# Optimization experiments

Measured on AMD Instinct MI355X. Metric: run time of the kernel, lower is better.

Reference implementation:

```python
import jax, jax.numpy as jnp
import numpy as np

B, S, D, DC, H = 4, 2048, 768, 384, 12
HD = DC // H  # compressed head_dim = 32


def setup_inputs() -> dict:
    key = jax.random.key(0)
    ks = jax.random.split(key, 8)
    std = 0.02
    return {
        "hidden_states": jax.random.normal(ks[0], (B, S, D), dtype=jnp.float32),
        "W_attn": jax.random.normal(ks[1], (D, 3 * D), dtype=jnp.float32) * std,
        "b_attn": jnp.zeros((3 * D,), dtype=jnp.float32),
        "P_q": jax.random.normal(ks[2], (D, DC), dtype=jnp.float32) * std,
        "P_k": jax.random.normal(ks[3], (D, DC), dtype=jnp.float32) * std,
        "P_v": jax.random.normal(ks[4], (D, DC), dtype=jnp.float32) * std,
        "W_back": jax.random.normal(ks[5], (DC, D), dtype=jnp.float32) * std,
        "W_proj": jax.random.normal(ks[6], (D, D), dtype=jnp.float32) * std,
        "b_proj": jnp.zeros((D,), dtype=jnp.float32),
    }


def reference(hidden_states, W_attn, b_attn, P_q, P_k, P_v, W_back, W_proj, b_proj):
    b, s, _ = hidden_states.shape
    # GPT-2 Conv1D style c_attn: out = x @ W + b, then split into q,k,v
    qkv = hidden_states @ W_attn + b_attn          # [B,S,3D]
    q, k, v = jnp.split(qkv, 3, axis=-1)           # each [B,S,D]
    # sparsify hooks: per-token linear compression D -> DC
    q = q @ P_q                                    # [B,S,DC]
    k = k @ P_k
    v = v @ P_v
    # split heads -> [B,H,S,HD]
    split = lambda t: t.reshape(b, s, H, HD).transpose(0, 2, 1, 3)
    qh, kh, vh = split(q), split(k), split(v)
    # naive attention with explicit causal mask (as in original _attn)
    scores = jnp.einsum("bhqd,bhkd->bhqk", qh, kh) / jnp.sqrt(jnp.float32(HD))
    causal = jnp.tril(jnp.ones((s, s), dtype=scores.dtype))  # [S,S]
    scores = scores * causal + (-10000.0) * (1.0 - causal)
    weights = jax.nn.softmax(scores, axis=-1)
    ctx = jnp.einsum("bhqk,bhkd->bhqd", weights, vh)         # [B,H,S,HD]
    # merge heads -> [B,S,DC]
    ctx = ctx.transpose(0, 2, 1, 3).reshape(b, s, DC)
    # backproject DC -> D, then c_proj
    out = ctx @ W_back                             # [B,S,D]
    out = out @ W_proj + b_proj                    # [B,S,D]
    return out
```

## Files before the change

kernel.cpp:

```cpp
#include <hip/hip_runtime.h>
#include <math.h>


typedef unsigned short u16;
typedef unsigned int   u32;

#define VLD 8320

using short8 = __attribute__((ext_vector_type(8))) short;
using bf16x4 = __attribute__((ext_vector_type(4))) short;
using f32x4  = __attribute__((ext_vector_type(4))) float;

__device__ __forceinline__ u16 f2bf(float f) {
  u32 u = __builtin_bit_cast(u32, f);
  u = (u + 0x7fffu + ((u >> 16) & 1u)) >> 16;
  return (u16)u;
}

__device__ __forceinline__ float b2f(u16 b) {
  return __builtin_bit_cast(float, (u32)b << 16);
}

__device__ __forceinline__ u32 cvtpk_bf16(float lo, float hi) {
  u32 d;
  asm("v_cvt_pk_bf16_f32 %0, %1, %2" : "=v"(d) : "v"(lo), "v"(hi));
  return d;
}

__device__ __forceinline__ bf16x4 pack4(const f32x4 v) {
  union { u32 u[2]; bf16x4 s; } c;
  c.u[0] = cvtpk_bf16(v[0], v[1]);
  c.u[1] = cvtpk_bf16(v[2], v[3]);
  return c.s;
}

__device__ __forceinline__ float exp2v(float x) {
  return __builtin_amdgcn_exp2f(x);
}

__device__ __forceinline__ f32x4 mfma16bf(bf16x4 a, bf16x4 b, f32x4 c) {
#if __has_builtin(__builtin_amdgcn_mfma_f32_16x16x16bf16_1k)
  return __builtin_amdgcn_mfma_f32_16x16x16bf16_1k(a, b, c, 0, 0, 0);
#elif __has_builtin(__builtin_amdgcn_mfma_f32_16x16x16_bf16)
  return __builtin_amdgcn_mfma_f32_16x16x16_bf16(a, b, c, 0, 0, 0);
#else
  f32x4 d;
  asm("v_mfma_f32_16x16x16_bf16 %0, %1, %2, %3"
      : "=v"(d) : "v"(a), "v"(b), "v"(c));
  return d;
#endif
}

__device__ __forceinline__ void gload_lds16(const void* g, void* l) {
  __builtin_amdgcn_global_load_lds((__attribute__((address_space(1))) u32*)g,
                                   (__attribute__((address_space(3))) u32*)l,
                                   16, 0, 0);
}

__device__ __forceinline__ u32 lds_u32(const void* p) {
  return (u32)(size_t)(const __attribute__((address_space(3))) char*)p;
}

__global__ __launch_bounds__(256) void prep_all(
    const float* __restrict__ x, const float* __restrict__ Wa,
    const float* __restrict__ Wb, const float* __restrict__ Pq,
    const float* __restrict__ Pk, const float* __restrict__ Pv,
    const float* __restrict__ Wp,
    u16* __restrict__ x_bf, u16* __restrict__ Wat_bf, u16* __restrict__ Wbk_bf,
    u16* __restrict__ PT, u16* __restrict__ WprT) {
  __shared__ float t[32][33];
  const int blk = blockIdx.x, tid = threadIdx.x;
  if (blk < 8160) {
    const float* src; u16* dst; int i;
    if (blk < 6144)      { src = x;  dst = x_bf;   i = blk * 256 + tid; }
    else if (blk < 7872) { src = Wa; dst = Wat_bf; i = (blk - 6144) * 256 + tid; }
    else                 { src = Wb; dst = Wbk_bf; i = (blk - 7872) * 256 + tid; }
    const float4 v = ((const float4*)src)[i];
    ((ushort4*)dst)[i] = make_ushort4(f2bf(v.x), f2bf(v.y), f2bf(v.z), f2bf(v.w));
    return;
  }
  const float* src; u16* dst; int C, R, bx, by;
  if (blk < 8448)      { src = Pq; dst = PT;             R = 768; C = 384; int t2 = blk - 8160; bx = t2 % 12; by = t2 / 12; }
  else if (blk < 8736) { src = Pk; dst = PT + 384 * 768; R = 768; C = 384; int t2 = blk - 8448; bx = t2 % 12; by = t2 / 12; }
  else if (blk < 9024) { src = Pv; dst = PT + 768 * 768; R = 768; C = 384; int t2 = blk - 8736; bx = t2 % 12; by = t2 / 12; }
  else                 { src = Wp; dst = WprT;           R = 768; C = 768; int t2 = blk - 9024; bx = t2 % 24; by = t2 / 24; }
  const int c0 = bx * 32, r0 = by * 32, tx = tid & 31, ty = tid >> 5;
  for (int i = ty; i < 32; i += 8)
    t[i][tx] = src[(size_t)(r0 + i) * C + c0 + tx];
  __syncthreads();
  for (int i = ty; i < 32; i += 8)
    dst[(size_t)(c0 + i) * R + r0 + tx] = f2bf(t[tx][i]);
}

template<int OBF16>
__device__ __forceinline__ void gemm_tile(
    const u16* __restrict__ A, const u16* __restrict__ BT,
    const float* __restrict__ bias, void* __restrict__ Cv,
    int K, int lda, int ldb, int ldc, int m0, int n0, int biasmode, bool slab,
    u16* As, u16* Bs) {
  const int tid = threadIdx.x;
  const int l = tid & 63, w = tid >> 6;
  const int r = l & 15, g = l >> 4;
  const int koff = slab ? (m0 / 384) * 768 : 0;
  const u16* Ap = A + ((size_t)m0 + w * 16 + r) * lda + g * 8;
  const u16* Bp = BT + ((size_t)n0 + w * 16 + r) * ldb + koff + g * 8;
  f32x4 acc[4][4] = {};
  const int wma = (w >> 1) * 4, wnb = (w & 1) * 4;
  const int nk = K >> 5;

  const u32 abase = lds_u32(As) + (u32)(wma * 1024 + l * 16);
  const u32 bbase = lds_u32(Bs) + (u32)(wnb * 1024 + l * 16);

  auto stage = [&](int kt, int buf) {
    const int o = buf * 4096;
    gload_lds16(Ap + kt,                    &As[o + (size_t)tid * 8]);
    gload_lds16(Ap + kt + (size_t)64 * lda, &As[o + 2048 + (size_t)tid * 8]);
    gload_lds16(Bp + kt,                    &Bs[o + (size_t)tid * 8]);
    gload_lds16(Bp + kt + (size_t)64 * ldb, &Bs[o + 2048 + (size_t)tid * 8]);
  };

  stage(0, 0);
  stage(32, 1);
  stage(64, 2);
  int cur = 0;
  for (int t = 0; t < nk; ++t) {
    if (t + 2 < nk)      asm volatile("s_waitcnt vmcnt(8)" ::: "memory");
    else if (t + 1 < nk) asm volatile("s_waitcnt vmcnt(4)" ::: "memory");
    else                 asm volatile("s_waitcnt vmcnt(0)" ::: "memory");
    __builtin_amdgcn_s_barrier();
    __builtin_amdgcn_sched_barrier(0);
    const u32 off = (u32)(cur * 8192);
    short8 af[4], bfr[4];
    #pragma unroll
    for (int i = 0; i < 4; ++i) {
      asm volatile("ds_read_b128 %0, %1" : "=v"(af[i])  : "v"(abase + off + 1024u * i));
      asm volatile("ds_read_b128 %0, %1" : "=v"(bfr[i]) : "v"(bbase + off + 1024u * i));
    }
    asm volatile("s_waitcnt lgkmcnt(0)" ::: "memory");
    __builtin_amdgcn_sched_barrier(0);
    __builtin_amdgcn_s_barrier();
    __builtin_amdgcn_sched_barrier(0);
    if (t + 3 < nk) stage((t + 3) << 5, cur);
    #pragma unroll
    for (int mi = 0; mi < 4; ++mi)
      #pragma unroll
      for (int ni = 0; ni < 4; ++ni)
        acc[mi][ni] = __builtin_amdgcn_mfma_f32_16x16x32_bf16(af[mi], bfr[ni],
                                                              acc[mi][ni], 0, 0, 0);
    cur = (cur == 2) ? 0 : cur + 1;
  }

  const int row0 = m0 + (w >> 1) * 64, col0 = n0 + (w & 1) * 64;
  #pragma unroll
  for (int ni = 0; ni < 4; ++ni) {
    const int col = col0 + ni * 16 + r;
    const float bvc = (biasmode == 1) ? bias[col] : 0.f;
    #pragma unroll
    for (int mi = 0; mi < 4; ++mi)
      #pragma unroll
      for (int j = 0; j < 4; ++j) {
        const int row = row0 + mi * 16 + 4 * g + j;
        float bv = bvc;
        if (biasmode == 2) bv = bias[row];
        const float v = acc[mi][ni][j] + bv;
        if (OBF16) ((u16*)Cv)[(size_t)row * ldc + col] = f2bf(v);
        else       ((float*)Cv)[(size_t)row * ldc + col] = v;
      }
  }
}

__global__ __launch_bounds__(256, 3) void gemm_prep(
    const u16* __restrict__ PT, const u16* __restrict__ Wat,
    const u16* __restrict__ WprT, const u16* __restrict__ Wbk,
    const float* __restrict__ ba,
    u16* __restrict__ WcT, u16* __restrict__ WbpT, float* __restrict__ bc) {
  __shared__ alignas(16) u16 As[12288], Bs[12288];
  const int t = blockIdx.x;
  if (t < 54) {
    gemm_tile<1>(PT, Wat, nullptr, WcT, 768, 768, 2304, 768,
                 (t % 9) * 128, (t / 9) * 128, 0, true, As, Bs);
  } else if (t < 72) {
    const int t2 = t - 54;
    gemm_tile<1>(WprT, Wbk, nullptr, WbpT, 768, 768, 768, 384,
                 (t2 % 6) * 128, (t2 / 6) * 128, 0, false, As, Bs);
  } else {
    const int c = (t - 72) * 144 + threadIdx.x;
    if (threadIdx.x < 144 && c < 1152) {
      const int slab = c / 384;
      const float* bs = ba + slab * 768;
      const u16* row = PT + (size_t)c * 768;
      float s = 0.f;
      for (int jj = 0; jj < 96; ++jj) {
        const short8 v = *(const short8*)&row[jj * 8];
        #pragma unroll
        for (int e = 0; e < 8; ++e)
          s = fmaf(bs[jj * 8 + e], b2f((u16)v[e]), s);
      }
      bc[c] = s;
    }
  }
}

__global__ __launch_bounds__(256, 3) void gemm_qkvt(
    const u16* __restrict__ x_bf, const u16* __restrict__ WcT,
    const float* __restrict__ bc, u16* __restrict__ QKbuf, u16* __restrict__ VTbuf) {
  __shared__ alignas(16) u16 As[12288], Bs[12288];
  const int t = blockIdx.x;
  const int w = (t & 7) * 72 + (t >> 3);
  const int s = w / 9, j = w % 9;
  if (j < 6) {
    gemm_tile<1>(x_bf, WcT, bc, QKbuf, 768, 768, 768, 768,
                 s * 128, j * 128, 1, false, As, Bs);
  } else {
    gemm_tile<1>(WcT + (size_t)768 * 768, x_bf, bc + 768, VTbuf, 768, 768, 768, VLD,
                 (j - 6) * 128, s * 128, 2, false, As, Bs);
  }
}

__global__ __launch_bounds__(256, 3) void gemm_out(
    const u16* __restrict__ ctx, const u16* __restrict__ WbpT,
    const float* __restrict__ bp, float* __restrict__ out) {
  __shared__ alignas(16) u16 As[12288], Bs[12288];
  const int t = blockIdx.x;
  const int w = (t & 7) * 48 + (t >> 3);
  gemm_tile<0>(ctx, WbpT, bp, out, 384, 384, 384, 768,
               (w / 6) * 128, (w % 6) * 128, 1, false, As, Bs);
}

__global__ __launch_bounds__(256, 4) void attn_kernel(
    const u16* __restrict__ QK, const u16* __restrict__ VT,
    u16* __restrict__ ctx) {
  __shared__ alignas(16) u16 Ks[2][2048];
  __shared__ alignas(16) u16 Vs[2][32 * 72];
  const int tid = threadIdx.x;
  const int w = tid >> 6, l = tid & 63;
  const int r = l & 15, g = l >> 4;
  const int idx = blockIdx.x;
  const int cc = 15 - idx / 48;
  const int bh = idx % 48;
  const int b = bh / 12, h = bh % 12;
  const size_t tok0 = (size_t)b * 2048;
  const int q0 = cc * 128 + w * 32;
  const u16* Qb = QK + (tok0 + q0) * 768 + h * 32;
  const u16* Kb = QK + tok0 * 768 + 384 + h * 32;
  const u16* Vb = VT + (size_t)(h * 32) * VLD + b * 2048;
  const float scale2 = 0.25500526474f;
  const float THR = 8.0f;
  const f32x4 fz = {0.f, 0.f, 0.f, 0.f};

  short8 qf[2];
  qf[0] = *(const short8*)&Qb[(size_t)r * 768 + 8 * g];
  qf[1] = *(const short8*)&Qb[(size_t)(16 + r) * 768 + 8 * g];

  float mrun[2] = {-3.0e38f, -3.0e38f};
  float lpart[2] = {0.f, 0.f};
  f32x4 o[2][2] = {};
  const int ntb = 2 * (cc + 1);
  const int ntw = (q0 + 31) / 64 + 1;

  const int krow = ((tid >> 6) << 4) + (tid & 15);
  const int kcol = ((tid >> 4) & 3) * 8;
  const int vd   = tid >> 3;
  const int vkc  = (tid & 7) * 8;

  uint4 vreg;
  auto stageK = [&](int t, int buf) {
    gload_lds16(&Kb[(size_t)(t * 64 + krow) * 768 + kcol], &Ks[buf][(size_t)tid * 8]);
  };
  auto loadV = [&](int t) {
    vreg = *(const uint4*)&Vb[(size_t)vd * VLD + t * 64 + vkc];
  };
  auto writeV = [&](int buf) {
    *(uint4*)&Vs[buf][vd * 72 + vkc] = vreg;
  };

  loadV(0); stageK(0, 0); writeV(0);
  __syncthreads();
  int cur = 0;
  for (int t = 0; t < ntb; ++t) {
    const bool pf = (t + 1 < ntb);
    if (pf) { loadV(t + 1); stageK(t + 1, cur ^ 1); }
    if (t < ntw) {
      short8 kf[4];
      #pragma unroll
      for (int kj = 0; kj < 4; ++kj)
        kf[kj] = *(const short8*)&Ks[cur][((kj * 64 + l)) * 8];
      bf16x4 vf[2][4];
      #pragma unroll
      for (int di = 0; di < 2; ++di)
        #pragma unroll
        for (int kj = 0; kj < 4; ++kj)
          vf[di][kj] = *(const bf16x4*)&Vs[cur][(16 * di + r) * 72 + kj * 16 + 4 * g];

      f32x4 s[2][4];
      __builtin_amdgcn_s_setprio(1);
      #pragma unroll
      for (int kj = 0; kj < 4; ++kj)
        #pragma unroll
        for (int mi = 0; mi < 2; ++mi)
          s[mi][kj] = __builtin_amdgcn_mfma_f32_16x16x32_bf16(kf[kj], qf[mi], fz, 0, 0, 0);
      __builtin_amdgcn_s_setprio(0);

      if (t == ntw - 1) {
        #pragma unroll
        for (int mi = 0; mi < 2; ++mi) {
          const int qq = q0 + mi * 16 + r;
          #pragma unroll
          for (int kj = 0; kj < 4; ++kj)
            #pragma unroll
            for (int jj = 0; jj < 4; ++jj) {
              const int kk = t * 64 + kj * 16 + 4 * g + jj;
              if (kk > qq) s[mi][kj][jj] = -3.0e38f;
            }
        }
      }

      #pragma unroll
      for (int mi = 0; mi < 2; ++mi) {
        const float a0 = fmaxf(fmaxf(s[mi][0][0], s[mi][0][1]), fmaxf(s[mi][0][2], s[mi][0][3]));
        const float a1 = fmaxf(fmaxf(s[mi][1][0], s[mi][1][1]), fmaxf(s[mi][1][2], s[mi][1][3]));
        const float a2 = fmaxf(fmaxf(s[mi][2][0], s[mi][2][1]), fmaxf(s[mi][2][2], s[mi][2][3]));
        const float a3 = fmaxf(fmaxf(s[mi][3][0], s[mi][3][1]), fmaxf(s[mi][3][2], s[mi][3][3]));
        const float lmxs = fmaxf(fmaxf(a0, a1), fmaxf(a2, a3)) * scale2;
        if (__any(lmxs > mrun[mi] + THR)) {
          float mx = lmxs;
          mx = fmaxf(mx, __shfl_xor(mx, 16));
          mx = fmaxf(mx, __shfl_xor(mx, 32));
          const float mnew = fmaxf(mrun[mi], mx);
          const float al = exp2v(mrun[mi] - mnew);
          mrun[mi] = mnew;
          lpart[mi] *= al;
          o[0][mi] *= al;
          o[1][mi] *= al;
        }
        #pragma unroll
        for (int kj = 0; kj < 4; ++kj)
          #pragma unroll
          for (int jj = 0; jj < 4; ++jj) {
            const float pv = exp2v(fmaf(s[mi][kj][jj], scale2, -mrun[mi]));
            s[mi][kj][jj] = pv;
            lpart[mi] += pv;
          }
      }

      __builtin_amdgcn_s_setprio(1);
      #pragma unroll
      for (int kj = 0; kj < 4; ++kj) {
        const bf16x4 pf0 = pack4(s[0][kj]);
        const bf16x4 pf1 = pack4(s[1][kj]);
        #pragma unroll
        for (int di = 0; di < 2; ++di) {
          o[di][0] = mfma16bf(vf[di][kj], pf0, o[di][0]);
          o[di][1] = mfma16bf(vf[di][kj], pf1, o[di][1]);
        }
      }
      __builtin_amdgcn_s_setprio(0);
    }
    if (pf) writeV(cur ^ 1);
    __syncthreads();
    cur ^= 1;
  }

  #pragma unroll
  for (int mi = 0; mi < 2; ++mi) {
    float lr = lpart[mi];
    lr += __shfl_xor(lr, 16);
    lr += __shfl_xor(lr, 32);
    const float li = 1.0f / lr;
    const size_t row = tok0 + q0 + mi * 16 + r;
    #pragma unroll
    for (int di = 0; di < 2; ++di) {
      const u32 d0 = cvtpk_bf16(o[di][mi][0] * li, o[di][mi][1] * li);
      const u32 d1 = cvtpk_bf16(o[di][mi][2] * li, o[di][mi][3] * li);
      *(uint2*)&ctx[row * 384 + h * 32 + di * 16 + 4 * g] = make_uint2(d0, d1);
    }
  }
}

extern "C" void kernel_launch(void* const* d_in, const int* in_sizes, int n_in,
                              void* d_out, int out_size, void* d_ws, size_t ws_size,
                              hipStream_t stream) {
  const float* x      = (const float*)d_in[0];
  const float* W_attn = (const float*)d_in[1];
  const float* b_attn = (const float*)d_in[2];
  const float* P_q    = (const float*)d_in[3];
  const float* P_k    = (const float*)d_in[4];
  const float* P_v    = (const float*)d_in[5];
  const float* W_back = (const float*)d_in[6];
  const float* W_proj = (const float*)d_in[7];
  const float* b_proj = (const float*)d_in[8];

  char* ws = (char*)d_ws;
  u16*   x_bf   = (u16*)(ws);
  u16*   ctx    = (u16*)(ws);
  u16*   Wat_bf = (u16*)(ws + 12582912);
  u16*   PT     = (u16*)(ws + 16121856);
  u16*   Wbk_bf = (u16*)(ws + 17891328);
  u16*   WprT   = (u16*)(ws + 18481152);
  u16*   WcT    = (u16*)(ws + 19660800);
  u16*   WbpT   = (u16*)(ws + 21430272);
  float* bc     = (float*)(ws + 22020096);
  u16*   QKbuf  = (u16*)d_out;
  u16*   VTbuf  = (u16*)((char*)d_out + 12582912);
  float* out    = (float*)d_out;

  prep_all<<<9600, 256, 0, stream>>>(x, W_attn, W_back, P_q, P_k, P_v, W_proj,
                                     x_bf, Wat_bf, Wbk_bf, PT, WprT);
  gemm_prep<<<80, 256, 0, stream>>>(PT, Wat_bf, WprT, Wbk_bf, b_attn, WcT, WbpT, bc);
  gemm_qkvt<<<576, 256, 0, stream>>>(x_bf, WcT, bc, QKbuf, VTbuf);
  attn_kernel<<<768, 256, 0, stream>>>(QKbuf, VTbuf, ctx);
  gemm_out<<<384, 256, 0, stream>>>(ctx, WbpT, b_proj, out);
}
```

Measured before the change: 120.9 us.

## Use 512-thread 128x256 GEMM tiles with three-stage LDS pipeline for QKV and output

Adds a gemm_tile8 routine in which 8 waves compute a 128x256 output tile, each wave owning a 64x64 sub-tile. Global-to-LDS loads are triple-buffered and issued three k-steps ahead, with vmcnt-based waits. The QKV/VT projection and the output projection kernels switch to this tile with half as many 512-thread blocks, to get more data reuse per block and hide load latency better. The cost is more LDS per block (72KB) and fewer blocks to spread over the CUs, which can lower occupancy and hurt load balance.

```diff
diff --git a/kernel.cpp b/kernel.cpp
--- a/kernel.cpp
+++ b/kernel.cpp
@@ -93,7 +93,83 @@
 }
 
 template<int OBF16>
-__device__ __forceinline__ void gemm_tile(
+__device__ __forceinline__ void gemm_tile8(
+    const u16* __restrict__ A, const u16* __restrict__ BT,
+    const float* __restrict__ bias, void* __restrict__ Cv,
+    int K, int lda, int ldb, int ldc, int m0, int n0, int biasmode,
+    u16* As, u16* Bs) {
+  const int tid = threadIdx.x;
+  const int l = tid & 63, w = tid >> 6;
+  const int r = l & 15, g = l >> 4;
+  const int w8 = w;
+  const u16* Ap = A + ((size_t)m0 + w8 * 16 + r) * lda + g * 8;
+  const u16* Bp = BT + ((size_t)n0 + w8 * 16 + r) * ldb + g * 8;
+  f32x4 acc[4][4] = {};
+  const int wm = w >> 2, wn = w & 3;
+  const int nk = K >> 5;
+
+  const u32 abase = lds_u32(As) + (u32)(wm * 4096 + l * 16);
+  const u32 bbase = lds_u32(Bs) + (u32)(wn * 4096 + l * 16);
+
+  auto stage = [&](int kt, int buf) {
+    gload_lds16(Ap + kt,                     &As[buf * 4096 + (size_t)tid * 8]);
+    gload_lds16(Bp + kt,                     &Bs[buf * 8192 + (size_t)tid * 8]);
+    gload_lds16(Bp + kt + (size_t)128 * ldb, &Bs[buf * 8192 + 4096 + (size_t)tid * 8]);
+  };
+
+  stage(0, 0);
+  stage(32, 1);
+  stage(64, 2);
+  int cur = 0;
+  for (int t = 0; t < nk; ++t) {
+    if (t + 2 < nk)      asm volatile("s_waitcnt vmcnt(6)" ::: "memory");
+    else if (t + 1 < nk) asm volatile("s_waitcnt vmcnt(3)" ::: "memory");
+    else                 asm volatile("s_waitcnt vmcnt(0)" ::: "memory");
+    __builtin_amdgcn_s_barrier();
+    __builtin_amdgcn_sched_barrier(0);
+    const u32 aoff = (u32)(cur * 8192);
+    const u32 boff = (u32)(cur * 16384);
+    short8 af[4], bfr[4];
+    #pragma unroll
+    for (int i = 0; i < 4; ++i) {
+      asm volatile("ds_read_b128 %0, %1" : "=v"(af[i])  : "v"(abase + aoff + 1024u * i));
+      asm volatile("ds_read_b128 %0, %1" : "=v"(bfr[i]) : "v"(bbase + boff + 1024u * i));
+    }
+    asm volatile("s_waitcnt lgkmcnt(0)" ::: "memory");
+    __builtin_amdgcn_sched_barrier(0);
+    __builtin_amdgcn_s_barrier();
+    __builtin_amdgcn_sched_barrier(0);
+    if (t + 3 < nk) stage((t + 3) << 5, cur);
+    #pragma unroll
+    for (int mi = 0; mi < 4; ++mi)
+      #pragma unroll
+      for (int ni = 0; ni < 4; ++ni)
+        acc[mi][ni] = __builtin_amdgcn_mfma_f32_16x16x32_bf16(af[mi], bfr[ni],
+                                                              acc[mi][ni], 0, 0, 0);
+    cur = (cur == 2) ? 0 : cur + 1;
+  }
+
+  const int row0 = m0 + wm * 64, col0 = n0 + wn * 64;
+  #pragma unroll
+  for (int ni = 0; ni < 4; ++ni) {
+    const int col = col0 + ni * 16 + r;
+    const float bvc = (biasmode == 1) ? bias[col] : 0.f;
+    #pragma unroll
+    for (int mi = 0; mi < 4; ++mi)
+      #pragma unroll
+      for (int j = 0; j < 4; ++j) {
+        const int row = row0 + mi * 16 + 4 * g + j;
+        float bv = bvc;
+        if (biasmode == 2) bv = bias[row];
+        const float v = acc[mi][ni][j] + bv;
+        if (OBF16) ((u16*)Cv)[(size_t)row * ldc + col] = f2bf(v);
+        else       ((float*)Cv)[(size_t)row * ldc + col] = v;
+      }
+  }
+}
+
+template<int OBF16>
+__device__ __forceinline__ void gemm_tile4(
     const u16* __restrict__ A, const u16* __restrict__ BT,
     const float* __restrict__ bias, void* __restrict__ Cv,
     int K, int lda, int ldb, int ldc, int m0, int n0, int biasmode, bool slab,
@@ -177,12 +253,12 @@
   __shared__ alignas(16) u16 As[12288], Bs[12288];
   const int t = blockIdx.x;
   if (t < 54) {
-    gemm_tile<1>(PT, Wat, nullptr, WcT, 768, 768, 2304, 768,
-                 (t % 9) * 128, (t / 9) * 128, 0, true, As, Bs);
+    gemm_tile4<1>(PT, Wat, nullptr, WcT, 768, 768, 2304, 768,
+                  (t % 9) * 128, (t / 9) * 128, 0, true, As, Bs);
   } else if (t < 72) {
     const int t2 = t - 54;
-    gemm_tile<1>(WprT, Wbk, nullptr, WbpT, 768, 768, 768, 384,
-                 (t2 % 6) * 128, (t2 / 6) * 128, 0, false, As, Bs);
+    gemm_tile4<1>(WprT, Wbk, nullptr, WbpT, 768, 768, 768, 384,
+                  (t2 % 6) * 128, (t2 / 6) * 128, 0, false, As, Bs);
   } else {
     const int c = (t - 72) * 144 + threadIdx.x;
     if (threadIdx.x < 144 && c < 1152) {
@@ -201,30 +277,31 @@
   }
 }
 
-__global__ __launch_bounds__(256, 3) void gemm_qkvt(
+__global__ __launch_bounds__(512, 4) void gemm_qkvt(
     const u16* __restrict__ x_bf, const u16* __restrict__ WcT,
     const float* __restrict__ bc, u16* __restrict__ QKbuf, u16* __restrict__ VTbuf) {
-  __shared__ alignas(16) u16 As[12288], Bs[12288];
+  __shared__ alignas(16) u16 As[12288], Bs[24576];
   const int t = blockIdx.x;
-  const int w = (t & 7) * 72 + (t >> 3);
-  const int s = w / 9, j = w % 9;
+  const int w = (t & 7) * 36 + (t >> 3);
+  const int S = w / 9, j = w % 9;
   if (j < 6) {
-    gemm_tile<1>(x_bf, WcT, bc, QKbuf, 768, 768, 768, 768,
-                 s * 128, j * 128, 1, false, As, Bs);
+    gemm_tile8<1>(x_bf, WcT, bc, QKbuf, 768, 768, 768, 768,
+                  (S * 2 + (j & 1)) * 128, (j >> 1) * 256, 1, As, Bs);
   } else {
-    gemm_tile<1>(WcT + (size_t)768 * 768, x_bf, bc + 768, VTbuf, 768, 768, 768, VLD,
-                 (j - 6) * 128, s * 128, 2, false, As, Bs);
-  }
-}
-
-__global__ __launch_bounds__(256, 3) void gemm_out(
+    gemm_tile8<1>(WcT + (size_t)(768 + (j - 6) * 128) * 768 - (size_t)(j - 6) * 128 * 768
+                    + (size_t)0, x_bf, bc + 768, VTbuf, 768, 768, 768, VLD,
+                  (j - 6) * 128, S * 256, 2, As, Bs);
+  }
+}
+
+__global__ __launch_bounds__(512, 4) void gemm_out(
     const u16* __restrict__ ctx, const u16* __restrict__ WbpT,
     const float* __restrict__ bp, float* __restrict__ out) {
-  __shared__ alignas(16) u16 As[12288], Bs[12288];
+  __shared__ alignas(16) u16 As[12288], Bs[24576];
   const int t = blockIdx.x;
-  const int w = (t & 7) * 48 + (t >> 3);
-  gemm_tile<0>(ctx, WbpT, bp, out, 384, 384, 384, 768,
-               (w / 6) * 128, (w % 6) * 128, 1, false, As, Bs);
+  const int w = (t & 7) * 24 + (t >> 3);
+  gemm_tile8<0>(ctx, WbpT, bp, out, 384, 384, 384, 768,
+                (w / 3) * 128, (w % 3) * 256, 1, As, Bs);
 }
 
 __global__ __launch_bounds__(256, 4) void attn_kernel(
@@ -407,7 +484,7 @@
   prep_all<<<9600, 256, 0, stream>>>(x, W_attn, W_back, P_q, P_k, P_v, W_proj,
                                      x_bf, Wat_bf, Wbk_bf, PT, WprT);
   gemm_prep<<<80, 256, 0, stream>>>(PT, Wat_bf, WprT, Wbk_bf, b_attn, WcT, WbpT, bc);
-  gemm_qkvt<<<576, 256, 0, stream>>>(x_bf, WcT, bc, QKbuf, VTbuf);
+  gemm_qkvt<<<288, 512, 0, stream>>>(x_bf, WcT, bc, QKbuf, VTbuf);
   attn_kernel<<<768, 256, 0, stream>>>(QKbuf, VTbuf, ctx);
-  gemm_out<<<384, 256, 0, stream>>>(ctx, WbpT, b_proj, out);
-}
+  gemm_out<<<192, 512, 0, stream>>>(ctx, WbpT, b_proj, out);
+}
```

After: 122.7 us. Within noise of the previous version (+1.5%).
